# Kernel tuning notes

Measured on AMD Instinct MI355X. Metric: run time of the kernel, lower is better.

## Reference

```python
import jax, jax.numpy as jnp
import numpy as np


def setup_inputs() -> dict:
    key = jax.random.key(0)
    k1, k2, k3, k4 = jax.random.split(key, 4)
    B, T, S, D = 256, 16, 32, 768
    return {
        "video_global": jax.random.normal(k1, (B, D), dtype=jnp.float32),
        "text_global": jax.random.normal(k2, (B, D), dtype=jnp.float32),
        "video_local": jax.random.normal(k3, (B, T, D), dtype=jnp.float32),
        "text_local": jax.random.normal(k4, (B, S, D), dtype=jnp.float32),
        "temp": jnp.zeros((1,), dtype=jnp.float32),  # log(1.0)
    }


def reference(video_global, text_global, video_local, text_local, temp):
    B = video_global.shape[0]
    logit_scale = jnp.exp(temp)[0]

    # ---- global contrastive loss ----
    global_sim = logit_scale * (video_global @ text_global.T)  # [B, B]
    diag = jnp.arange(B)
    loss_v2t = -jax.nn.log_softmax(global_sim, axis=1)[diag, diag].mean()
    loss_t2v = -jax.nn.log_softmax(global_sim, axis=0)[diag, diag].mean()
    loss_global = 0.5 * (loss_v2t + loss_t2v)

    # ---- local positive scores ----
    # paired (diagonal) local similarity: [B, T, S]
    sim_pos = logit_scale * jnp.einsum("btd,bsd->bts", video_local, text_local)
    time_weights = jax.nn.softmax(sim_pos.max(axis=-1), axis=-1)  # [B, T]
    pos_scores = (sim_pos.mean(axis=-1) * time_weights).sum(axis=1)  # [B]

    # ---- local negative scores (batched pairwise contraction) ----
    # [B, B, T, S]: video i vs text j, replacing the B*(B-1) tiny einsum loop
    sim_all = logit_scale * jnp.einsum("btd,csd->bcts", video_local, text_local)
    neg_full = (time_weights[:, None, :] * sim_all.mean(axis=-1)).sum(axis=-1)  # [B, B]

    # drop diagonal (i == j), preserving row-major loop order
    rows, cols = np.nonzero(~np.eye(B, dtype=bool))
    neg_scores = neg_full[rows, cols].reshape(B, B - 1)

    logits = jnp.concatenate([pos_scores[:, None], neg_scores], axis=-1)  # [B, B]
    loss_local = -jax.nn.log_softmax(logits, axis=-1)[:, 0].mean()

    return 0.6 * loss_global + 0.4 * loss_local
```

## Files before the change

kernel.cpp:

```cpp
#include <hip/hip_runtime.h>
#include <cmath>

#define BB 256
#define TT 16
#define SS 32
#define DD 768
#define LROW 260

__global__ __launch_bounds__(512) void hl_stage1(
    const float* __restrict__ vl, const float* __restrict__ tl,
    const float* __restrict__ temp,
    float* __restrict__ vw_ws, float* __restrict__ tb_ws)
{
    __shared__ float smem[12480];
    __shared__ float simb[512];
    __shared__ float rmax[16];
    __shared__ float twb[16];

    const int i   = blockIdx.x;
    const int tid = threadIdx.x;
    const float lsc = expf(temp[0]);

    const int slice = tid & 15;
    const int g     = tid >> 4;
    const int tg    = g >> 3;
    const int sg    = g & 7;

    const float* vli = vl + (size_t)i * TT * DD;
    const float* tli = tl + (size_t)i * SS * DD;

    float acc[4][4];
#pragma unroll
    for (int a = 0; a < 4; ++a)
#pragma unroll
        for (int b = 0; b < 4; ++b) acc[a][b] = 0.f;

    for (int c = 0; c < 3; ++c) {
        const int d0 = c << 8;
#pragma unroll
        for (int k = 0; k < 2; ++k) {
            int f4 = tid + (k << 9);
            int r  = f4 >> 6;
            int q  = f4 & 63;
            int pq = q ^ ((q >> 3) & 7);
            *(float4*)&smem[r * LROW + (pq << 2)] =
                *(const float4*)&vli[r * DD + d0 + (q << 2)];
        }
#pragma unroll
        for (int k = 0; k < 4; ++k) {
            int f4 = tid + (k << 9);
            int r  = f4 >> 6;
            int q  = f4 & 63;
            int pq = q ^ ((q >> 3) & 7);
            *(float4*)&smem[(16 + r) * LROW + (pq << 2)] =
                *(const float4*)&tli[r * DD + d0 + (q << 2)];
        }
        __syncthreads();
#pragma unroll
        for (int step = 0; step < 4; ++step) {
            const int db = (((slice << 2) + step) ^ (slice >> 1)) << 2;
            float4 av[4], bv[4];
#pragma unroll
            for (int ti = 0; ti < 4; ++ti)
                av[ti] = *(const float4*)&smem[(tg * 4 + ti) * LROW + db];
#pragma unroll
            for (int sj = 0; sj < 4; ++sj)
                bv[sj] = *(const float4*)&smem[(16 + sg * 4 + sj) * LROW + db];
#pragma unroll
            for (int ti = 0; ti < 4; ++ti)
#pragma unroll
                for (int sj = 0; sj < 4; ++sj)
                    acc[ti][sj] += av[ti].x * bv[sj].x + av[ti].y * bv[sj].y
                                 + av[ti].z * bv[sj].z + av[ti].w * bv[sj].w;
        }
        __syncthreads();
    }

#pragma unroll
    for (int ti = 0; ti < 4; ++ti)
#pragma unroll
        for (int sj = 0; sj < 4; ++sj) {
            int t = tg * 4 + ti, s = sg * 4 + sj;
            smem[(t * 32 + s) * 17 + slice] = acc[ti][sj];
        }
    __syncthreads();
    {
        float ssum = 0.f;
#pragma unroll
        for (int k = 0; k < 16; ++k) ssum += smem[tid * 17 + k];
        simb[tid] = lsc * ssum;
    }
    __syncthreads();
    if (tid < 16) {
        float m = -3.0e38f;
        for (int s = 0; s < 32; ++s)
            m = fmaxf(m, simb[tid * 32 + ((s + tid) & 31)]);
        rmax[tid] = m;
    }
    __syncthreads();
    if (tid == 0) {
        float M = -3.0e38f;
        for (int t = 0; t < 16; ++t) M = fmaxf(M, rmax[t]);
        float ssum = 0.f;
        for (int t = 0; t < 16; ++t) {
            float e = expf(rmax[t] - M);
            twb[t] = e;
            ssum += e;
        }
        float inv = 1.0f / ssum;
        for (int t = 0; t < 16; ++t) twb[t] *= inv;
    }
    __syncthreads();

    for (int d = tid; d < DD; d += 512) {
        float vwv = 0.f;
#pragma unroll
        for (int t = 0; t < 16; ++t) vwv += twb[t] * vli[t * DD + d];
        vw_ws[(size_t)i * DD + d] = vwv;
        float tbv = 0.f;
#pragma unroll
        for (int s = 0; s < 32; ++s) tbv += tli[s * DD + d];
        tb_ws[(size_t)i * DD + d] = tbv * (1.0f / 32.0f);
    }
}

__global__ __launch_bounds__(256) void hl_gemm(
    const float* __restrict__ vg, const float* __restrict__ tg,
    const float* __restrict__ vw, const float* __restrict__ tb,
    const float* __restrict__ temp, float* __restrict__ cparts)
{
    __shared__ float As[16][68];
    __shared__ float Bs[16][68];
    __shared__ float Tb[64][68];

    const int b   = blockIdx.x;
    const int p   = b & 7;
    const int tj  = (b >> 3) & 3;
    const int ti  = (b >> 5) & 3;
    const int mat = b >> 7;
    const int tid = threadIdx.x;
    const float lsc = expf(temp[0]);

    const float* A  = mat ? vw : vg;
    const float* Bm = mat ? tb : tg;
    const int i0 = ti * 64, j0 = tj * 64, kb0 = p * 96;

    const int srow = tid >> 2, skq = tid & 3;
    const int tr = tid >> 4, tc = tid & 15;

    float acc[4][4];
#pragma unroll
    for (int r = 0; r < 4; ++r)
#pragma unroll
        for (int cc = 0; cc < 4; ++cc) acc[r][cc] = 0.f;

    for (int ch = 0; ch < 6; ++ch) {
        const int kb = kb0 + ch * 16;
        float4 a4 = *(const float4*)&A [(size_t)(i0 + srow) * DD + kb + skq * 4];
        float4 b4 = *(const float4*)&Bm[(size_t)(j0 + srow) * DD + kb + skq * 4];
        __syncthreads();
        As[skq * 4 + 0][srow] = a4.x; As[skq * 4 + 1][srow] = a4.y;
        As[skq * 4 + 2][srow] = a4.z; As[skq * 4 + 3][srow] = a4.w;
        Bs[skq * 4 + 0][srow] = b4.x; Bs[skq * 4 + 1][srow] = b4.y;
        Bs[skq * 4 + 2][srow] = b4.z; Bs[skq * 4 + 3][srow] = b4.w;
        __syncthreads();
#pragma unroll
        for (int k = 0; k < 16; ++k) {
            float4 av = *(const float4*)&As[k][tr * 4];
            float4 bv = *(const float4*)&Bs[k][tc * 4];
            float ar[4] = {av.x, av.y, av.z, av.w};
            float br[4] = {bv.x, bv.y, bv.z, bv.w};
#pragma unroll
            for (int r = 0; r < 4; ++r)
#pragma unroll
                for (int cc = 0; cc < 4; ++cc)
                    acc[r][cc] += ar[r] * br[cc];
        }
    }

    const int cm = mat ? 0 : 1;
    float* Cp = cparts + ((size_t)p * 3 + cm) * 65536;
#pragma unroll
    for (int r = 0; r < 4; ++r) {
        float4 v = {acc[r][0] * lsc, acc[r][1] * lsc, acc[r][2] * lsc, acc[r][3] * lsc};
        *(float4*)&Cp[(size_t)(i0 + tr * 4 + r) * 256 + j0 + tc * 4] = v;
    }
    if (mat == 0) {
        __syncthreads();
#pragma unroll
        for (int r = 0; r < 4; ++r)
#pragma unroll
            for (int cc = 0; cc < 4; ++cc)
                Tb[tc * 4 + cc][tr * 4 + r] = acc[r][cc] * lsc;
        __syncthreads();
        float* Ct = cparts + ((size_t)p * 3 + 2) * 65536;
#pragma unroll
        for (int r = 0; r < 4; ++r) {
            float4 v = *(const float4*)&Tb[tr * 4 + r][tc * 4];
            *(float4*)&Ct[(size_t)(j0 + tr * 4 + r) * 256 + i0 + tc * 4] = v;
        }
    }
}

__global__ __launch_bounds__(256) void hl_lse(
    const float* __restrict__ cparts, float* __restrict__ out)
{
    __shared__ float xs[256];
    __shared__ float wred[4];
    __shared__ float bcast;

    const int b   = blockIdx.x;
    const int cm  = b >> 8;
    const int row = b & 255;
    const int tid = threadIdx.x;

    float x = 0.f;
#pragma unroll
    for (int p = 0; p < 8; ++p)
        x += cparts[((size_t)p * 3 + cm) * 65536 + (size_t)row * 256 + tid];
    xs[tid] = x;

    float m = x;
#pragma unroll
    for (int off = 32; off > 0; off >>= 1)
        m = fmaxf(m, __shfl_down(m, off, 64));
    if ((tid & 63) == 0) wred[tid >> 6] = m;
    __syncthreads();
    if (tid == 0)
        bcast = fmaxf(fmaxf(wred[0], wred[1]), fmaxf(wred[2], wred[3]));
    __syncthreads();
    float M = bcast;
    float e = expf(x - M);
#pragma unroll
    for (int off = 32; off > 0; off >>= 1)
        e += __shfl_down(e, off, 64);
    if ((tid & 63) == 0) wred[tid >> 6] = e;
    __syncthreads();
    if (tid == 0) {
        float Stot = wred[0] + wred[1] + wred[2] + wred[3];
        float lse  = M + logf(Stot);
        float w    = (cm == 0) ? (0.4f / 256.0f) : (0.3f / 256.0f);
        atomicAdd(out, w * (lse - xs[row]));
    }
}

extern "C" void kernel_launch(void* const* d_in, const int* in_sizes, int n_in,
                              void* d_out, int out_size, void* d_ws, size_t ws_size,
                              hipStream_t stream)
{
    const float* vg   = (const float*)d_in[0];
    const float* tg   = (const float*)d_in[1];
    const float* vl   = (const float*)d_in[2];
    const float* tl   = (const float*)d_in[3];
    const float* temp = (const float*)d_in[4];
    float* out = (float*)d_out;

    float* vw     = (float*)d_ws;
    float* tb     = vw + (size_t)BB * DD;
    float* cparts = tb + (size_t)BB * DD;

    hipMemsetAsync(out, 0, sizeof(float) * out_size, stream);
    hl_stage1<<<dim3(BB),  dim3(512), 0, stream>>>(vl, tl, temp, vw, tb);
    hl_gemm  <<<dim3(256), dim3(256), 0, stream>>>(vg, tg, vw, tb, temp, cparts);
    hl_lse   <<<dim3(768), dim3(256), 0, stream>>>(cparts, out);
}
```

Measured before the change: 115.5 us.

## Fold global GEMM and output zeroing into stage-1 kernel

Moves the global video-text GEMM (mat 0) out of the second kernel and runs it as a tail phase of the first 128 blocks of the stage-1 kernel, reusing the same shared memory. The output memset is replaced by block 0 zeroing the output inside that kernel. The second kernel now computes only the local matrix with 128 blocks. This removes one memset launch and halves the dependent GEMM launch, but adds a serial tail to some stage-1 blocks and leaves half the threads of those blocks idle during it.

```diff
diff --git a/kernel.cpp b/kernel.cpp
--- a/kernel.cpp
+++ b/kernel.cpp
@@ -7,144 +7,228 @@
 #define DD 768
 #define LROW 260
 
-__global__ __launch_bounds__(512) void hl_stage1(
+__global__ __launch_bounds__(512) void hl_k1(
+    const float* __restrict__ vg, const float* __restrict__ tg,
     const float* __restrict__ vl, const float* __restrict__ tl,
     const float* __restrict__ temp,
-    float* __restrict__ vw_ws, float* __restrict__ tb_ws)
+    float* __restrict__ vw_ws, float* __restrict__ tb_ws,
+    float* __restrict__ cparts, float* __restrict__ out, int out_n)
 {
-    __shared__ float smem[12480];
-    __shared__ float simb[512];
-    __shared__ float rmax[16];
-    __shared__ float twb[16];
-
-    const int i   = blockIdx.x;
+    __shared__ float lds[13024];
     const int tid = threadIdx.x;
     const float lsc = expf(temp[0]);
 
-    const int slice = tid & 15;
-    const int g     = tid >> 4;
-    const int tg    = g >> 3;
-    const int sg    = g & 7;
-
-    const float* vli = vl + (size_t)i * TT * DD;
-    const float* tli = tl + (size_t)i * SS * DD;
-
-    float acc[4][4];
-#pragma unroll
-    for (int a = 0; a < 4; ++a)
-#pragma unroll
-        for (int b = 0; b < 4; ++b) acc[a][b] = 0.f;
-
-    for (int c = 0; c < 3; ++c) {
-        const int d0 = c << 8;
-#pragma unroll
-        for (int k = 0; k < 2; ++k) {
-            int f4 = tid + (k << 9);
-            int r  = f4 >> 6;
-            int q  = f4 & 63;
-            int pq = q ^ ((q >> 3) & 7);
-            *(float4*)&smem[r * LROW + (pq << 2)] =
-                *(const float4*)&vli[r * DD + d0 + (q << 2)];
-        }
-#pragma unroll
-        for (int k = 0; k < 4; ++k) {
-            int f4 = tid + (k << 9);
-            int r  = f4 >> 6;
-            int q  = f4 & 63;
-            int pq = q ^ ((q >> 3) & 7);
-            *(float4*)&smem[(16 + r) * LROW + (pq << 2)] =
-                *(const float4*)&tli[r * DD + d0 + (q << 2)];
-        }
-        __syncthreads();
-#pragma unroll
-        for (int step = 0; step < 4; ++step) {
-            const int db = (((slice << 2) + step) ^ (slice >> 1)) << 2;
-            float4 av[4], bv[4];
-#pragma unroll
-            for (int ti = 0; ti < 4; ++ti)
-                av[ti] = *(const float4*)&smem[(tg * 4 + ti) * LROW + db];
-#pragma unroll
-            for (int sj = 0; sj < 4; ++sj)
-                bv[sj] = *(const float4*)&smem[(16 + sg * 4 + sj) * LROW + db];
-#pragma unroll
-            for (int ti = 0; ti < 4; ++ti)
+    {
+        float* smem = lds;
+        float* simb = lds + 12480;
+        float* rmax = lds + 12992;
+        float* twb  = lds + 13008;
+        const int i = blockIdx.x;
+
+        if (i == 0) {
+            for (int o = tid; o < out_n; o += 512) out[o] = 0.f;
+        }
+
+        const int slice = tid & 15;
+        const int g     = tid >> 4;
+        const int tg_   = g >> 3;
+        const int sg    = g & 7;
+
+        const float* vli = vl + (size_t)i * TT * DD;
+        const float* tli = tl + (size_t)i * SS * DD;
+
+        float acc[4][4];
+#pragma unroll
+        for (int a = 0; a < 4; ++a)
+#pragma unroll
+            for (int b = 0; b < 4; ++b) acc[a][b] = 0.f;
+
+        for (int c = 0; c < 3; ++c) {
+            const int d0 = c << 8;
+#pragma unroll
+            for (int k = 0; k < 2; ++k) {
+                int f4 = tid + (k << 9);
+                int r  = f4 >> 6;
+                int q  = f4 & 63;
+                int pq = q ^ ((q >> 3) & 7);
+                *(float4*)&smem[r * LROW + (pq << 2)] =
+                    *(const float4*)&vli[r * DD + d0 + (q << 2)];
+            }
+#pragma unroll
+            for (int k = 0; k < 4; ++k) {
+                int f4 = tid + (k << 9);
+                int r  = f4 >> 6;
+                int q  = f4 & 63;
+                int pq = q ^ ((q >> 3) & 7);
+                *(float4*)&smem[(16 + r) * LROW + (pq << 2)] =
+                    *(const float4*)&tli[r * DD + d0 + (q << 2)];
+            }
+            __syncthreads();
+#pragma unroll
+            for (int step = 0; step < 4; ++step) {
+                const int db = (((slice << 2) + step) ^ (slice >> 1)) << 2;
+                float4 av[4], bv[4];
+#pragma unroll
+                for (int ti = 0; ti < 4; ++ti)
+                    av[ti] = *(const float4*)&smem[(tg_ * 4 + ti) * LROW + db];
 #pragma unroll
                 for (int sj = 0; sj < 4; ++sj)
-                    acc[ti][sj] += av[ti].x * bv[sj].x + av[ti].y * bv[sj].y
-                                 + av[ti].z * bv[sj].z + av[ti].w * bv[sj].w;
-        }
-        __syncthreads();
-    }
-
-#pragma unroll
-    for (int ti = 0; ti < 4; ++ti)
-#pragma unroll
-        for (int sj = 0; sj < 4; ++sj) {
-            int t = tg * 4 + ti, s = sg * 4 + sj;
-            smem[(t * 32 + s) * 17 + slice] = acc[ti][sj];
-        }
-    __syncthreads();
-    {
-        float ssum = 0.f;
-#pragma unroll
-        for (int k = 0; k < 16; ++k) ssum += smem[tid * 17 + k];
-        simb[tid] = lsc * ssum;
-    }
-    __syncthreads();
-    if (tid < 16) {
-        float m = -3.0e38f;
-        for (int s = 0; s < 32; ++s)
-            m = fmaxf(m, simb[tid * 32 + ((s + tid) & 31)]);
-        rmax[tid] = m;
-    }
-    __syncthreads();
-    if (tid == 0) {
-        float M = -3.0e38f;
-        for (int t = 0; t < 16; ++t) M = fmaxf(M, rmax[t]);
-        float ssum = 0.f;
-        for (int t = 0; t < 16; ++t) {
-            float e = expf(rmax[t] - M);
-            twb[t] = e;
-            ssum += e;
-        }
-        float inv = 1.0f / ssum;
-        for (int t = 0; t < 16; ++t) twb[t] *= inv;
-    }
-    __syncthreads();
-
-    for (int d = tid; d < DD; d += 512) {
-        float vwv = 0.f;
-#pragma unroll
-        for (int t = 0; t < 16; ++t) vwv += twb[t] * vli[t * DD + d];
-        vw_ws[(size_t)i * DD + d] = vwv;
-        float tbv = 0.f;
-#pragma unroll
-        for (int s = 0; s < 32; ++s) tbv += tli[s * DD + d];
-        tb_ws[(size_t)i * DD + d] = tbv * (1.0f / 32.0f);
+                    bv[sj] = *(const float4*)&smem[(16 + sg * 4 + sj) * LROW + db];
+#pragma unroll
+                for (int ti = 0; ti < 4; ++ti)
+#pragma unroll
+                    for (int sj = 0; sj < 4; ++sj)
+                        acc[ti][sj] += av[ti].x * bv[sj].x + av[ti].y * bv[sj].y
+                                     + av[ti].z * bv[sj].z + av[ti].w * bv[sj].w;
+            }
+            __syncthreads();
+        }
+
+#pragma unroll
+        for (int ti = 0; ti < 4; ++ti)
+#pragma unroll
+            for (int sj = 0; sj < 4; ++sj) {
+                int t = tg_ * 4 + ti, s = sg * 4 + sj;
+                smem[(t * 32 + s) * 17 + slice] = acc[ti][sj];
+            }
+        __syncthreads();
+        {
+            float ssum = 0.f;
+#pragma unroll
+            for (int k = 0; k < 16; ++k) ssum += smem[tid * 17 + k];
+            simb[tid] = lsc * ssum;
+        }
+        __syncthreads();
+        if (tid < 16) {
+            float m = -3.0e38f;
+            for (int s = 0; s < 32; ++s)
+                m = fmaxf(m, simb[tid * 32 + ((s + tid) & 31)]);
+            rmax[tid] = m;
+        }
+        __syncthreads();
+        if (tid == 0) {
+            float M = -3.0e38f;
+            for (int t = 0; t < 16; ++t) M = fmaxf(M, rmax[t]);
+            float ssum = 0.f;
+            for (int t = 0; t < 16; ++t) {
+                float e = expf(rmax[t] - M);
+                twb[t] = e;
+                ssum += e;
+            }
+            float inv = 1.0f / ssum;
+            for (int t = 0; t < 16; ++t) twb[t] *= inv;
+        }
+        __syncthreads();
+
+        for (int d = tid; d < DD; d += 512) {
+            float vwv = 0.f;
+#pragma unroll
+            for (int t = 0; t < 16; ++t) vwv += twb[t] * vli[t * DD + d];
+            vw_ws[(size_t)i * DD + d] = vwv;
+            float tbv = 0.f;
+#pragma unroll
+            for (int s = 0; s < 32; ++s) tbv += tli[s * DD + d];
+            tb_ws[(size_t)i * DD + d] = tbv * (1.0f / 32.0f);
+        }
+    }
+
+    if (blockIdx.x < 128) {
+        __syncthreads();
+        float (*As)[68] = (float (*)[68])lds;
+        float (*Bs)[68] = (float (*)[68])(lds + 1088);
+        float (*Tb)[68] = (float (*)[68])(lds + 2176);
+
+        const int b  = blockIdx.x;
+        const int p  = b & 7;
+        const int tj = (b >> 3) & 3;
+        const int ti = (b >> 5) & 3;
+        const int i0 = ti * 64, j0 = tj * 64, kb0 = p * 96;
+
+        const bool act = tid < 256;
+        const int srow = tid >> 2, skq = tid & 3;
+        const int tr = tid >> 4, tc = tid & 15;
+
+        float acc[4][4];
+#pragma unroll
+        for (int r = 0; r < 4; ++r)
+#pragma unroll
+            for (int cc = 0; cc < 4; ++cc) acc[r][cc] = 0.f;
+
+        for (int ch = 0; ch < 6; ++ch) {
+            const int kb = kb0 + ch * 16;
+            float4 a4, b4;
+            if (act) {
+                a4 = *(const float4*)&vg[(size_t)(i0 + srow) * DD + kb + skq * 4];
+                b4 = *(const float4*)&tg[(size_t)(j0 + srow) * DD + kb + skq * 4];
+            }
+            __syncthreads();
+            if (act) {
+                As[skq * 4 + 0][srow] = a4.x; As[skq * 4 + 1][srow] = a4.y;
+                As[skq * 4 + 2][srow] = a4.z; As[skq * 4 + 3][srow] = a4.w;
+                Bs[skq * 4 + 0][srow] = b4.x; Bs[skq * 4 + 1][srow] = b4.y;
+                Bs[skq * 4 + 2][srow] = b4.z; Bs[skq * 4 + 3][srow] = b4.w;
+            }
+            __syncthreads();
+            if (act) {
+#pragma unroll
+                for (int k = 0; k < 16; ++k) {
+                    float4 av = *(const float4*)&As[k][tr * 4];
+                    float4 bv = *(const float4*)&Bs[k][tc * 4];
+                    float ar[4] = {av.x, av.y, av.z, av.w};
+                    float br[4] = {bv.x, bv.y, bv.z, bv.w};
+#pragma unroll
+                    for (int r = 0; r < 4; ++r)
+#pragma unroll
+                        for (int cc = 0; cc < 4; ++cc)
+                            acc[r][cc] += ar[r] * br[cc];
+                }
+            }
+        }
+
+        if (act) {
+            float* Cp = cparts + ((size_t)p * 3 + 1) * 65536;
+#pragma unroll
+            for (int r = 0; r < 4; ++r) {
+                float4 v = {acc[r][0] * lsc, acc[r][1] * lsc,
+                            acc[r][2] * lsc, acc[r][3] * lsc};
+                *(float4*)&Cp[(size_t)(i0 + tr * 4 + r) * 256 + j0 + tc * 4] = v;
+            }
+        }
+        __syncthreads();
+        if (act) {
+#pragma unroll
+            for (int r = 0; r < 4; ++r)
+#pragma unroll
+                for (int cc = 0; cc < 4; ++cc)
+                    Tb[tc * 4 + cc][tr * 4 + r] = acc[r][cc] * lsc;
+        }
+        __syncthreads();
+        if (act) {
+            float* Ct = cparts + ((size_t)p * 3 + 2) * 65536;
+#pragma unroll
+            for (int r = 0; r < 4; ++r) {
+                float4 v = *(const float4*)&Tb[tr * 4 + r][tc * 4];
+                *(float4*)&Ct[(size_t)(j0 + tr * 4 + r) * 256 + i0 + tc * 4] = v;
+            }
+        }
     }
 }
 
-__global__ __launch_bounds__(256) void hl_gemm(
-    const float* __restrict__ vg, const float* __restrict__ tg,
+__global__ __launch_bounds__(256) void hl_gemm_m1(
     const float* __restrict__ vw, const float* __restrict__ tb,
     const float* __restrict__ temp, float* __restrict__ cparts)
 {
     __shared__ float As[16][68];
     __shared__ float Bs[16][68];
-    __shared__ float Tb[64][68];
 
     const int b   = blockIdx.x;
     const int p   = b & 7;
     const int tj  = (b >> 3) & 3;
     const int ti  = (b >> 5) & 3;
-    const int mat = b >> 7;
     const int tid = threadIdx.x;
     const float lsc = expf(temp[0]);
 
-    const float* A  = mat ? vw : vg;
-    const float* Bm = mat ? tb : tg;
     const int i0 = ti * 64, j0 = tj * 64, kb0 = p * 96;
-
     const int srow = tid >> 2, skq = tid & 3;
     const int tr = tid >> 4, tc = tid & 15;
 
@@ -156,8 +240,8 @@
 
     for (int ch = 0; ch < 6; ++ch) {
         const int kb = kb0 + ch * 16;
-        float4 a4 = *(const float4*)&A [(size_t)(i0 + srow) * DD + kb + skq * 4];
-        float4 b4 = *(const float4*)&Bm[(size_t)(j0 + srow) * DD + kb + skq * 4];
+        float4 a4 = *(const float4*)&vw[(size_t)(i0 + srow) * DD + kb + skq * 4];
+        float4 b4 = *(const float4*)&tb[(size_t)(j0 + srow) * DD + kb + skq * 4];
         __syncthreads();
         As[skq * 4 + 0][srow] = a4.x; As[skq * 4 + 1][srow] = a4.y;
         As[skq * 4 + 2][srow] = a4.z; As[skq * 4 + 3][srow] = a4.w;
@@ -178,27 +262,12 @@
         }
     }
 
-    const int cm = mat ? 0 : 1;
-    float* Cp = cparts + ((size_t)p * 3 + cm) * 65536;
+    float* Cp = cparts + (size_t)p * 3 * 65536;
 #pragma unroll
     for (int r = 0; r < 4; ++r) {
-        float4 v = {acc[r][0] * lsc, acc[r][1] * lsc, acc[r][2] * lsc, acc[r][3] * lsc};
+        float4 v = {acc[r][0] * lsc, acc[r][1] * lsc,
+                    acc[r][2] * lsc, acc[r][3] * lsc};
         *(float4*)&Cp[(size_t)(i0 + tr * 4 + r) * 256 + j0 + tc * 4] = v;
-    }
-    if (mat == 0) {
-        __syncthreads();
-#pragma unroll
-        for (int r = 0; r < 4; ++r)
-#pragma unroll
-            for (int cc = 0; cc < 4; ++cc)
-                Tb[tc * 4 + cc][tr * 4 + r] = acc[r][cc] * lsc;
-        __syncthreads();
-        float* Ct = cparts + ((size_t)p * 3 + 2) * 65536;
-#pragma unroll
-        for (int r = 0; r < 4; ++r) {
-            float4 v = *(const float4*)&Tb[tr * 4 + r][tc * 4];
-            *(float4*)&Ct[(size_t)(j0 + tr * 4 + r) * 256 + i0 + tc * 4] = v;
-        }
     }
 }
 
@@ -256,11 +325,11 @@
     float* out = (float*)d_out;
 
     float* vw     = (float*)d_ws;
-    float* tb     = vw + (size_t)BB * DD;
-    float* cparts = tb + (size_t)BB * DD;
-
-    hipMemsetAsync(out, 0, sizeof(float) * out_size, stream);
-    hl_stage1<<<dim3(BB),  dim3(512), 0, stream>>>(vl, tl, temp, vw, tb);
-    hl_gemm  <<<dim3(256), dim3(256), 0, stream>>>(vg, tg, vw, tb, temp, cparts);
-    hl_lse   <<<dim3(768), dim3(256), 0, stream>>>(cparts, out);
+    float* tbw    = vw + (size_t)BB * DD;
+    float* cparts = tbw + (size_t)BB * DD;
+
+    hl_k1     <<<dim3(BB),  dim3(512), 0, stream>>>(vg, tg, vl, tl, temp,
+                                                    vw, tbw, cparts, out, out_size);
+    hl_gemm_m1<<<dim3(128), dim3(256), 0, stream>>>(vw, tbw, temp, cparts);
+    hl_lse    <<<dim3(768), dim3(256), 0, stream>>>(cparts, out);
 }
```

After: 118.0 us. 2.2% more time.
